# Kernel tuning notes

Hardware: AMD Instinct MI355X
Metric: run time of the kernel (lower is better)

The kernel has to match this reference:

```python
import jax, jax.numpy as jnp
import numpy as np

N, C_IN, H, W = 256, 256, 28, 28
D = 64        # prototype channel dim (prototype_shape[1])
P = 200       # num prototypes
NCLS = 10


def setup_inputs() -> dict:
    key = jax.random.key(0)
    ks = jax.random.split(key, 6)
    x = jax.random.normal(ks[0], (N, C_IN, H, W), dtype=jnp.float32)
    W1 = jax.random.normal(ks[1], (D, C_IN), dtype=jnp.float32) * 0.05
    b1 = jnp.zeros((D,), dtype=jnp.float32)
    W2 = jax.random.normal(ks[2], (D, D), dtype=jnp.float32) * 0.05
    b2 = jnp.zeros((D,), dtype=jnp.float32)
    prototypes = jax.random.uniform(ks[3], (P, D), dtype=jnp.float32)
    last_W = jax.random.normal(ks[4], (NCLS, P), dtype=jnp.float32) * 0.05
    last_b = jnp.zeros((NCLS,), dtype=jnp.float32)
    return {"x": x, "W1": W1, "b1": b1, "W2": W2, "b2": b2,
            "prototypes": prototypes, "last_W": last_W, "last_b": last_b}


def reference(x, W1, b1, W2, b2, prototypes, last_W, last_b):
    # add_on_layers: 1x1 conv -> relu -> 1x1 conv -> sigmoid (pointwise GEMMs)
    h = jax.nn.relu(jnp.einsum('nchw,oc->nohw', x, W1) + b1[None, :, None, None])
    f = jax.nn.sigmoid(jnp.einsum('nchw,oc->nohw', h, W2) + b2[None, :, None, None])
    # L2 convolution with 1x1 prototypes:
    # conv(x^2, ones) == channel sum of f^2, broadcast over P prototypes
    x2_patch_sum = jnp.sum(f * f, axis=1, keepdims=True)          # (N,1,H,W)
    xp = jnp.einsum('nchw,pc->nphw', f, prototypes)               # (N,P,H,W)
    p2 = jnp.sum(prototypes * prototypes, axis=1)[None, :, None, None]  # (1,P,1,1)
    distances = jax.nn.relu(x2_patch_sum - 2.0 * xp + p2)         # (N,P,H,W)
    # global min-pool over spatial dims (== -maxpool(-d) with full kernel)
    min_distances = jnp.min(distances, axis=(2, 3))               # (N,P)
    # paf == 'linear': similarity = -distance
    prototype_activations = -min_distances
    logits = prototype_activations @ last_W.T + last_b            # (N,NCLS)
    return (logits, min_distances)
```

## Files before the change

### kernel.cpp

```cpp
#include <hip/hip_runtime.h>
#include <hip/hip_bf16.h>

#define NIMG 256
#define CIN  256
#define PIX  784
#define DD   64
#define NP   200
#define NPP  208
#define NCLS 10

#define XS 264
#define HS 72

typedef __attribute__((ext_vector_type(8))) short bf16x8;
typedef __attribute__((ext_vector_type(4))) float f32x4;
typedef __attribute__((ext_vector_type(4))) unsigned int u32x4;
typedef __attribute__((ext_vector_type(2))) unsigned int u32x2;

__device__ __forceinline__ unsigned short f2bf(float f) {
    union { float f; unsigned int u; } v; v.f = f;
    unsigned int r = v.u + 0x7fffu + ((v.u >> 16) & 1u);
    return (unsigned short)(r >> 16);
}
__device__ __forceinline__ unsigned int pk2(float a, float b) {
    __hip_bfloat162 p = __float22bfloat162_rn(make_float2(a, b));
    return *(unsigned int*)&p;
}

#define MFMA(a, b, c) __builtin_amdgcn_mfma_f32_16x16x32_bf16((a), (b), (c), 0, 0, 0)

#define BARL() asm volatile("s_waitcnt lgkmcnt(0)\n\ts_barrier" ::: "memory")

__global__ __launch_bounds__(512, 2)
void proto_fused_kernel(const float* __restrict__ x,
                        const float* __restrict__ W1, const float* __restrict__ b1,
                        const float* __restrict__ W2, const float* __restrict__ b2,
                        const float* __restrict__ proto,
                        const float* __restrict__ lastW, const float* __restrict__ lastb,
                        float* __restrict__ out)
{
    __shared__ __align__(16) unsigned short xlds[64 * XS];
    __shared__ __align__(16) unsigned short w1lds[64 * XS];
    __shared__ __align__(16) unsigned short w2lds[64 * HS];
    __shared__ __align__(16) unsigned short htile[64 * HS];
    __shared__ __align__(16) unsigned short ftile[64 * HS];
    __shared__ float p2lds[NPP];
    __shared__ float s2lds[2][64];
    __shared__ float b1lds[DD], b2lds[DD];
    __shared__ unsigned int bmin[NPP];

    const int n    = blockIdx.x;
    const int t    = threadIdx.x;
    const int lane = t & 63;
    const int q    = lane >> 4;
    const int l15  = lane & 15;
    const int wave = t >> 6;
    const int s    = wave & 3;
    const int dh   = wave >> 2;
    const int dt0  = dh * 2, dt1 = dh * 2 + 1;

    const int p4   = ((t >> 2) & 15) * 4;
    const int c8i  = (t & 3) | ((t >> 6) << 2);
    const int c8   = c8i * 8;
    const float* xn = x + (size_t)n * CIN * PIX;

    float4 pf[8];
    auto load_tile = [&](int px0) {
        #pragma unroll
        for (int j = 0; j < 8; ++j) {
            const float* src = xn + (size_t)(c8 + j) * PIX + px0 + p4;
            float4 v;
            if (px0 + p4 + 3 < PIX) {
                v = *(const float4*)src;
            } else {
                v.x = (px0 + p4 + 0 < PIX) ? src[0] : 0.f;
                v.y = (px0 + p4 + 1 < PIX) ? src[1] : 0.f;
                v.z = (px0 + p4 + 2 < PIX) ? src[2] : 0.f;
                v.w = (px0 + p4 + 3 < PIX) ? src[3] : 0.f;
            }
            pf[j] = v;
        }
    };
    auto store_tile = [&]() {
        #pragma unroll
        for (int r = 0; r < 4; ++r) {
            u32x4 uv;
            uv.x = pk2(((const float*)&pf[0])[r], ((const float*)&pf[1])[r]);
            uv.y = pk2(((const float*)&pf[2])[r], ((const float*)&pf[3])[r]);
            uv.z = pk2(((const float*)&pf[4])[r], ((const float*)&pf[5])[r]);
            uv.w = pk2(((const float*)&pf[6])[r], ((const float*)&pf[7])[r]);
            *(u32x4*)&xlds[(p4 + r) * XS + c8] = uv;
        }
    };

    load_tile(0);

    {
        const float4* W1v = (const float4*)W1;
        #pragma unroll
        for (int i = 0; i < 8; ++i) {
            int j = t + i * 512;
            float4 v = W1v[j];
            u32x2 w;
            w.x = pk2(v.x, v.y); w.y = pk2(v.z, v.w);
            *(u32x2*)&w1lds[(j >> 6) * XS + (j & 63) * 4] = w;
        }
    }
    {
        const float4* W2v = (const float4*)W2;
        #pragma unroll
        for (int i = 0; i < 2; ++i) {
            int j = t + i * 512;
            float4 v = W2v[j];
            u32x2 w;
            w.x = pk2(v.x, v.y); w.y = pk2(v.z, v.w);
            *(u32x2*)&w2lds[(j >> 4) * HS + (j & 15) * 4] = w;
        }
    }
    if (t < DD) { b1lds[t] = b1[t]; b2lds[t] = b2[t]; }
    if (t < NPP) {
        float acc = 0.f;
        if (t < NP) {
            const float4* pp = (const float4*)(proto + t * DD);
            #pragma unroll
            for (int i = 0; i < 16; ++i) {
                float4 v = pp[i];
                acc += v.x * v.x + v.y * v.y + v.z * v.z + v.w * v.w;
            }
        }
        p2lds[t] = acc;
        bmin[t] = 0x7f800000u;
    }

    bf16x8 pb0[7], pb1[7];
    #pragma unroll
    for (int it = 0; it < 7; ++it) {
        int pt = dh + 2 * it;
        int p  = pt * 16 + l15;
        int pr = (p < NP) ? p : (NP - 1);
        const float4* src = (const float4*)(proto + (size_t)pr * DD + q * 8);
        float4 a = src[0], b = src[1];
        float4 c = src[8], d = src[9];
        union { u32x4 u; bf16x8 h; } cv0, cv1;
        cv0.u.x = pk2(a.x, a.y); cv0.u.y = pk2(a.z, a.w);
        cv0.u.z = pk2(b.x, b.y); cv0.u.w = pk2(b.z, b.w);
        cv1.u.x = pk2(c.x, c.y); cv1.u.y = pk2(c.z, c.w);
        cv1.u.z = pk2(d.x, d.y); cv1.u.w = pk2(d.z, d.w);
        pb0[it] = cv0.h; pb1[it] = cv1.h;
    }

    store_tile();
    load_tile(64);
    BARL();

    bf16x8 w1f0[8], w1f1[8];
    #pragma unroll
    for (int kk = 0; kk < 8; ++kk) {
        w1f0[kk] = *(const bf16x8*)&w1lds[(dt0 * 16 + l15) * XS + kk * 32 + q * 8];
        w1f1[kk] = *(const bf16x8*)&w1lds[(dt1 * 16 + l15) * XS + kk * 32 + q * 8];
    }
    bf16x8 w2f0[2], w2f1[2];
    #pragma unroll
    for (int kk = 0; kk < 2; ++kk) {
        w2f0[kk] = *(const bf16x8*)&w2lds[(dt0 * 16 + l15) * HS + kk * 32 + q * 8];
        w2f1[kk] = *(const bf16x8*)&w2lds[(dt1 * 16 + l15) * HS + kk * 32 + q * 8];
    }
    float p2r[7];
    #pragma unroll
    for (int it = 0; it < 7; ++it) {
        int pidx = (dh + 2 * it) * 16 + l15;
        p2r[it] = p2lds[pidx < NPP ? pidx : (NPP - 1)];
    }

    float rmin[7];
    #pragma unroll
    for (int it = 0; it < 7; ++it) rmin[it] = 1e30f;

    for (int tl = 0; tl < 13; ++tl) {
        const int px0 = tl * 64;

        {
            f32x4 acc0 = {0.f, 0.f, 0.f, 0.f}, acc1 = {0.f, 0.f, 0.f, 0.f};
            const int arow = (s * 16 + l15) * XS + q * 8;
            #pragma unroll
            for (int kk = 0; kk < 8; ++kk) {
                bf16x8 a = *(const bf16x8*)&xlds[arow + kk * 32];
                acc0 = MFMA(a, w1f0[kk], acc0);
                acc1 = MFMA(a, w1f1[kk], acc1);
            }
            #pragma unroll
            for (int r = 0; r < 4; ++r) {
                int prow = s * 16 + q * 4 + r;
                float h0 = fmaxf(acc0[r] + b1lds[dt0 * 16 + l15], 0.f);
                float h1 = fmaxf(acc1[r] + b1lds[dt1 * 16 + l15], 0.f);
                htile[prow * HS + dt0 * 16 + l15] = f2bf(h0);
                htile[prow * HS + dt1 * 16 + l15] = f2bf(h1);
            }
        }
        BARL();

        if (tl < 12) store_tile();
        if (tl < 11) load_tile((tl + 2) * 64);
        {
            f32x4 acc0 = {0.f, 0.f, 0.f, 0.f}, acc1 = {0.f, 0.f, 0.f, 0.f};
            const int arowH = (s * 16 + l15) * HS + q * 8;
            bf16x8 a0 = *(const bf16x8*)&htile[arowH];
            bf16x8 a1 = *(const bf16x8*)&htile[arowH + 32];
            acc0 = MFMA(a0, w2f0[0], acc0);
            acc0 = MFMA(a1, w2f0[1], acc0);
            acc1 = MFMA(a0, w2f1[0], acc1);
            acc1 = MFMA(a1, w2f1[1], acc1);
            #pragma unroll
            for (int r = 0; r < 4; ++r) {
                int prow = s * 16 + q * 4 + r;
                float z0 = acc0[r] + b2lds[dt0 * 16 + l15];
                float z1 = acc1[r] + b2lds[dt1 * 16 + l15];
                float f0 = __builtin_amdgcn_rcpf(1.0f + __builtin_amdgcn_exp2f(z0 * -1.44269504f));
                float f1 = __builtin_amdgcn_rcpf(1.0f + __builtin_amdgcn_exp2f(z1 * -1.44269504f));
                ftile[prow * HS + dt0 * 16 + l15] = f2bf(f0);
                ftile[prow * HS + dt1 * 16 + l15] = f2bf(f1);
                float v = f0 * f0 + f1 * f1;
                v += __shfl_xor(v, 1, 64);
                v += __shfl_xor(v, 2, 64);
                v += __shfl_xor(v, 4, 64);
                v += __shfl_xor(v, 8, 64);
                if (l15 == 0)
                    s2lds[dh][prow] = (px0 + prow < PIX) ? v : 1e30f;
            }
        }
        BARL();

        {
            const int arowF = (s * 16 + l15) * HS + q * 8;
            bf16x8 a0 = *(const bf16x8*)&ftile[arowF];
            bf16x8 a1 = *(const bf16x8*)&ftile[arowF + 32];
            float s2v[4];
            #pragma unroll
            for (int r = 0; r < 4; ++r) {
                int pl = s * 16 + q * 4 + r;
                s2v[r] = s2lds[0][pl] + s2lds[1][pl];
            }
            #pragma unroll
            for (int it = 0; it < 7; ++it) {
                f32x4 acc = {0.f, 0.f, 0.f, 0.f};
                acc = MFMA(a0, pb0[it], acc);
                acc = MFMA(a1, pb1[it], acc);
                float m = 1e30f;
                #pragma unroll
                for (int r = 0; r < 4; ++r) {
                    float dist = fmaxf(s2v[r] - 2.f * acc[r] + p2r[it], 0.f);
                    m = fminf(m, dist);
                }
                rmin[it] = fminf(rmin[it], m);
            }
        }
    }

    #pragma unroll
    for (int it = 0; it < 7; ++it) {
        int pt = dh + 2 * it;
        if (pt < 13) {
            float m = rmin[it];
            m = fminf(m, __shfl_xor(m, 16, 64));
            m = fminf(m, __shfl_xor(m, 32, 64));
            if (lane < 16) atomicMin(&bmin[pt * 16 + l15], __float_as_uint(m));
        }
    }
    BARL();

    if (t < NP) {
        out[NIMG * NCLS + (size_t)n * NP + t] = __uint_as_float(bmin[t]);
    }
    if (t < 320) {
        int c = t >> 5, j = t & 31;
        float acc = 0.f;
        for (int p = j; p < NP; p += 32)
            acc += __uint_as_float(bmin[p]) * lastW[c * NP + p];
        acc += __shfl_xor(acc, 1, 32);
        acc += __shfl_xor(acc, 2, 32);
        acc += __shfl_xor(acc, 4, 32);
        acc += __shfl_xor(acc, 8, 32);
        acc += __shfl_xor(acc, 16, 32);
        if (j == 0) out[(size_t)n * NCLS + c] = -acc + lastb[c];
    }
}

extern "C" void kernel_launch(void* const* d_in, const int* in_sizes, int n_in,
                              void* d_out, int out_size, void* d_ws, size_t ws_size,
                              hipStream_t stream) {
    const float* x     = (const float*)d_in[0];
    const float* W1    = (const float*)d_in[1];
    const float* b1    = (const float*)d_in[2];
    const float* W2    = (const float*)d_in[3];
    const float* b2    = (const float*)d_in[4];
    const float* proto = (const float*)d_in[5];
    const float* lastW = (const float*)d_in[6];
    const float* lastb = (const float*)d_in[7];
    float* out = (float*)d_out;

    proto_fused_kernel<<<dim3(NIMG), dim3(512), 0, stream>>>(
        x, W1, b1, W2, b2, proto, lastW, lastb, out);
}
```

Before: 307.2 us.

## Stage x tiles in 128-pixel double chunks and stream W1 fragments from LDS

The x staging buffer grows to two 64-pixel halves and each global prefetch now covers 128 pixels (16 float4 registers), stored every other sub-tile, so loads have a longer window to overlap compute. To free the registers this needs, the W1 MFMA fragments are no longer held in registers and are instead reread from LDS on every sub-tile. This adds LDS traffic and doubles the shared-memory footprint of xlds, which could hurt occupancy at two blocks per CU. It also leaves the stored half untouched until the next store, relying on barrier ordering between halves.

```diff
diff --git a/kernel.cpp b/kernel.cpp
--- a/kernel.cpp
+++ b/kernel.cpp
@@ -39,7 +39,7 @@
                         const float* __restrict__ lastW, const float* __restrict__ lastb,
                         float* __restrict__ out)
 {
-    __shared__ __align__(16) unsigned short xlds[64 * XS];
+    __shared__ __align__(16) unsigned short xlds[128 * XS];
     __shared__ __align__(16) unsigned short w1lds[64 * XS];
     __shared__ __align__(16) unsigned short w2lds[64 * HS];
     __shared__ __align__(16) unsigned short htile[64 * HS];
@@ -64,36 +64,44 @@
     const int c8   = c8i * 8;
     const float* xn = x + (size_t)n * CIN * PIX;
 
-    float4 pf[8];
-    auto load_tile = [&](int px0) {
+    float4 pf[16];
+    auto load_tile128 = [&](int h) {
+        const int px0 = h * 128;
         #pragma unroll
         for (int j = 0; j < 8; ++j) {
-            const float* src = xn + (size_t)(c8 + j) * PIX + px0 + p4;
-            float4 v;
-            if (px0 + p4 + 3 < PIX) {
-                v = *(const float4*)src;
-            } else {
-                v.x = (px0 + p4 + 0 < PIX) ? src[0] : 0.f;
-                v.y = (px0 + p4 + 1 < PIX) ? src[1] : 0.f;
-                v.z = (px0 + p4 + 2 < PIX) ? src[2] : 0.f;
-                v.w = (px0 + p4 + 3 < PIX) ? src[3] : 0.f;
-            }
-            pf[j] = v;
+            #pragma unroll
+            for (int half = 0; half < 2; ++half) {
+                const int base = px0 + half * 64 + p4;
+                const float* src = xn + (size_t)(c8 + j) * PIX + base;
+                float4 v;
+                if (base + 3 < PIX) {
+                    v = *(const float4*)src;
+                } else {
+                    v.x = (base + 0 < PIX) ? src[0] : 0.f;
+                    v.y = (base + 1 < PIX) ? src[1] : 0.f;
+                    v.z = (base + 2 < PIX) ? src[2] : 0.f;
+                    v.w = (base + 3 < PIX) ? src[3] : 0.f;
+                }
+                pf[j * 2 + half] = v;
+            }
         }
     };
-    auto store_tile = [&]() {
+    auto store_tile128 = [&]() {
         #pragma unroll
-        for (int r = 0; r < 4; ++r) {
-            u32x4 uv;
-            uv.x = pk2(((const float*)&pf[0])[r], ((const float*)&pf[1])[r]);
-            uv.y = pk2(((const float*)&pf[2])[r], ((const float*)&pf[3])[r]);
-            uv.z = pk2(((const float*)&pf[4])[r], ((const float*)&pf[5])[r]);
-            uv.w = pk2(((const float*)&pf[6])[r], ((const float*)&pf[7])[r]);
-            *(u32x4*)&xlds[(p4 + r) * XS + c8] = uv;
+        for (int half = 0; half < 2; ++half) {
+            #pragma unroll
+            for (int r = 0; r < 4; ++r) {
+                u32x4 uv;
+                uv.x = pk2(((const float*)&pf[0 + half])[r], ((const float*)&pf[2 + half])[r]);
+                uv.y = pk2(((const float*)&pf[4 + half])[r], ((const float*)&pf[6 + half])[r]);
+                uv.z = pk2(((const float*)&pf[8 + half])[r], ((const float*)&pf[10 + half])[r]);
+                uv.w = pk2(((const float*)&pf[12 + half])[r], ((const float*)&pf[14 + half])[r]);
+                *(u32x4*)&xlds[(half * 64 + p4 + r) * XS + c8] = uv;
+            }
         }
     };
 
-    load_tile(0);
+    load_tile128(0);
 
     {
         const float4* W1v = (const float4*)W1;
@@ -149,16 +157,10 @@
         pb0[it] = cv0.h; pb1[it] = cv1.h;
     }
 
-    store_tile();
-    load_tile(64);
+    store_tile128();
+    load_tile128(1);
     BARL();
 
-    bf16x8 w1f0[8], w1f1[8];
-    #pragma unroll
-    for (int kk = 0; kk < 8; ++kk) {
-        w1f0[kk] = *(const bf16x8*)&w1lds[(dt0 * 16 + l15) * XS + kk * 32 + q * 8];
-        w1f1[kk] = *(const bf16x8*)&w1lds[(dt1 * 16 + l15) * XS + kk * 32 + q * 8];
-    }
     bf16x8 w2f0[2], w2f1[2];
     #pragma unroll
     for (int kk = 0; kk < 2; ++kk) {
@@ -176,17 +178,23 @@
     #pragma unroll
     for (int it = 0; it < 7; ++it) rmin[it] = 1e30f;
 
-    for (int tl = 0; tl < 13; ++tl) {
-        const int px0 = tl * 64;
+    const int w1r0 = (dt0 * 16 + l15) * XS + q * 8;
+    const int w1r1 = (dt1 * 16 + l15) * XS + q * 8;
+
+    for (int st = 0; st < 13; ++st) {
+        const int px0   = st * 64;
+        const int rbase = (st & 1) * 64;
 
         {
             f32x4 acc0 = {0.f, 0.f, 0.f, 0.f}, acc1 = {0.f, 0.f, 0.f, 0.f};
-            const int arow = (s * 16 + l15) * XS + q * 8;
+            const int arow = (rbase + s * 16 + l15) * XS + q * 8;
             #pragma unroll
             for (int kk = 0; kk < 8; ++kk) {
-                bf16x8 a = *(const bf16x8*)&xlds[arow + kk * 32];
-                acc0 = MFMA(a, w1f0[kk], acc0);
-                acc1 = MFMA(a, w1f1[kk], acc1);
+                bf16x8 a  = *(const bf16x8*)&xlds[arow + kk * 32];
+                bf16x8 w0 = *(const bf16x8*)&w1lds[w1r0 + kk * 32];
+                bf16x8 w1v = *(const bf16x8*)&w1lds[w1r1 + kk * 32];
+                acc0 = MFMA(a, w0, acc0);
+                acc1 = MFMA(a, w1v, acc1);
             }
             #pragma unroll
             for (int r = 0; r < 4; ++r) {
@@ -199,8 +207,10 @@
         }
         BARL();
 
-        if (tl < 12) store_tile();
-        if (tl < 11) load_tile((tl + 2) * 64);
+        if (st & 1) {
+            store_tile128();
+            if (st <= 9) load_tile128((st >> 1) + 2);
+        }
         {
             f32x4 acc0 = {0.f, 0.f, 0.f, 0.f}, acc1 = {0.f, 0.f, 0.f, 0.f};
             const int arowH = (s * 16 + l15) * HS + q * 8;
```

Result: no change. 312.1 us (+1.6%).

## Double block to 1024 threads with four-wave D split and deeper x prefetch

Applied to the files above, without the earlier changes.

Each block now runs 16 waves instead of 8. Each wave owns one 16-channel D tile instead of two, and the prototype tiles are spread over four wave groups instead of two. The x tile load is split into a three-buffer, deeper register prefetch rotation. W2 fragments are loaded straight from global memory into registers, and W1 fragments are re-read from LDS every iteration to save registers. The aim is more latency hiding on each CU, since a 256-image grid gives one block per CU. The cost is extra LDS traffic, a wider barrier and some waves idling in the prototype stage.

```diff
diff --git a/kernel.cpp b/kernel.cpp
--- a/kernel.cpp
+++ b/kernel.cpp
@@ -31,7 +31,7 @@
 
 #define BARL() asm volatile("s_waitcnt lgkmcnt(0)\n\ts_barrier" ::: "memory")
 
-__global__ __launch_bounds__(512, 2)
+__global__ __launch_bounds__(1024)
 void proto_fused_kernel(const float* __restrict__ x,
                         const float* __restrict__ W1, const float* __restrict__ b1,
                         const float* __restrict__ W2, const float* __restrict__ b2,
@@ -41,11 +41,10 @@
 {
     __shared__ __align__(16) unsigned short xlds[64 * XS];
     __shared__ __align__(16) unsigned short w1lds[64 * XS];
-    __shared__ __align__(16) unsigned short w2lds[64 * HS];
     __shared__ __align__(16) unsigned short htile[64 * HS];
     __shared__ __align__(16) unsigned short ftile[64 * HS];
     __shared__ float p2lds[NPP];
-    __shared__ float s2lds[2][64];
+    __shared__ float s2lds[4][64];
     __shared__ float b1lds[DD], b2lds[DD];
     __shared__ unsigned int bmin[NPP];
 
@@ -56,65 +55,54 @@
     const int l15  = lane & 15;
     const int wave = t >> 6;
     const int s    = wave & 3;
-    const int dh   = wave >> 2;
-    const int dt0  = dh * 2, dt1 = dh * 2 + 1;
-
-    const int p4   = ((t >> 2) & 15) * 4;
-    const int c8i  = (t & 3) | ((t >> 6) << 2);
-    const int c8   = c8i * 8;
+    const int dt   = wave >> 2;
+
+    const int p4  = ((t >> 2) & 15) * 4;
+    const int c4i = (t & 3) | ((t >> 6) << 2);
+    const int c4  = c4i * 4;
     const float* xn = x + (size_t)n * CIN * PIX;
 
-    float4 pf[8];
-    auto load_tile = [&](int px0) {
+    auto load_st = [&](float4 (&pf)[4], int st) {
+        const int base = st * 64 + p4;
         #pragma unroll
-        for (int j = 0; j < 8; ++j) {
-            const float* src = xn + (size_t)(c8 + j) * PIX + px0 + p4;
+        for (int j = 0; j < 4; ++j) {
+            const float* src = xn + (size_t)(c4 + j) * PIX + base;
             float4 v;
-            if (px0 + p4 + 3 < PIX) {
+            if (base + 3 < PIX) {
                 v = *(const float4*)src;
             } else {
-                v.x = (px0 + p4 + 0 < PIX) ? src[0] : 0.f;
-                v.y = (px0 + p4 + 1 < PIX) ? src[1] : 0.f;
-                v.z = (px0 + p4 + 2 < PIX) ? src[2] : 0.f;
-                v.w = (px0 + p4 + 3 < PIX) ? src[3] : 0.f;
+                v.x = (base + 0 < PIX) ? src[0] : 0.f;
+                v.y = (base + 1 < PIX) ? src[1] : 0.f;
+                v.z = (base + 2 < PIX) ? src[2] : 0.f;
+                v.w = (base + 3 < PIX) ? src[3] : 0.f;
             }
             pf[j] = v;
         }
     };
-    auto store_tile = [&]() {
+    auto store_st = [&](float4 (&pf)[4]) {
         #pragma unroll
         for (int r = 0; r < 4; ++r) {
-            u32x4 uv;
-            uv.x = pk2(((const float*)&pf[0])[r], ((const float*)&pf[1])[r]);
-            uv.y = pk2(((const float*)&pf[2])[r], ((const float*)&pf[3])[r]);
-            uv.z = pk2(((const float*)&pf[4])[r], ((const float*)&pf[5])[r]);
-            uv.w = pk2(((const float*)&pf[6])[r], ((const float*)&pf[7])[r]);
-            *(u32x4*)&xlds[(p4 + r) * XS + c8] = uv;
+            u32x2 w;
+            w.x = pk2(((const float*)&pf[0])[r], ((const float*)&pf[1])[r]);
+            w.y = pk2(((const float*)&pf[2])[r], ((const float*)&pf[3])[r]);
+            *(u32x2*)&xlds[(p4 + r) * XS + c4] = w;
         }
     };
 
-    load_tile(0);
+    float4 pfA[4], pfB[4], pfC[4];
+    load_st(pfA, 0);
+    load_st(pfB, 1);
+    load_st(pfC, 2);
 
     {
         const float4* W1v = (const float4*)W1;
         #pragma unroll
-        for (int i = 0; i < 8; ++i) {
-            int j = t + i * 512;
+        for (int i = 0; i < 4; ++i) {
+            int j = t + i * 1024;
             float4 v = W1v[j];
             u32x2 w;
             w.x = pk2(v.x, v.y); w.y = pk2(v.z, v.w);
             *(u32x2*)&w1lds[(j >> 6) * XS + (j & 63) * 4] = w;
-        }
-    }
-    {
-        const float4* W2v = (const float4*)W2;
-        #pragma unroll
-        for (int i = 0; i < 2; ++i) {
-            int j = t + i * 512;
-            float4 v = W2v[j];
-            u32x2 w;
-            w.x = pk2(v.x, v.y); w.y = pk2(v.z, v.w);
-            *(u32x2*)&w2lds[(j >> 4) * HS + (j & 15) * 4] = w;
         }
     }
     if (t < DD) { b1lds[t] = b1[t]; b2lds[t] = b2[t]; }
@@ -132,10 +120,21 @@
         bmin[t] = 0x7f800000u;
     }
 
-    bf16x8 pb0[7], pb1[7];
-    #pragma unroll
-    for (int it = 0; it < 7; ++it) {
-        int pt = dh + 2 * it;
+    bf16x8 w2f[2];
+    #pragma unroll
+    for (int kk = 0; kk < 2; ++kk) {
+        const float4* src = (const float4*)(W2 + (size_t)(dt * 16 + l15) * DD + kk * 32 + q * 8);
+        float4 a = src[0], b = src[1];
+        union { u32x4 u; bf16x8 h; } cv;
+        cv.u.x = pk2(a.x, a.y); cv.u.y = pk2(a.z, a.w);
+        cv.u.z = pk2(b.x, b.y); cv.u.w = pk2(b.z, b.w);
+        w2f[kk] = cv.h;
+    }
+
+    bf16x8 pb0[4], pb1[4];
+    #pragma unroll
+    for (int it = 0; it < 4; ++it) {
+        int pt = dt + 4 * it;
         int p  = pt * 16 + l15;
         int pr = (p < NP) ? p : (NP - 1);
         const float4* src = (const float4*)(proto + (size_t)pr * DD + q * 8);
@@ -149,116 +148,108 @@
         pb0[it] = cv0.h; pb1[it] = cv1.h;
     }
 
-    store_tile();
-    load_tile(64);
+    store_st(pfA);
+    load_st(pfA, 3);
     BARL();
 
-    bf16x8 w1f0[8], w1f1[8];
-    #pragma unroll
-    for (int kk = 0; kk < 8; ++kk) {
-        w1f0[kk] = *(const bf16x8*)&w1lds[(dt0 * 16 + l15) * XS + kk * 32 + q * 8];
-        w1f1[kk] = *(const bf16x8*)&w1lds[(dt1 * 16 + l15) * XS + kk * 32 + q * 8];
-    }
-    bf16x8 w2f0[2], w2f1[2];
-    #pragma unroll
-    for (int kk = 0; kk < 2; ++kk) {
-        w2f0[kk] = *(const bf16x8*)&w2lds[(dt0 * 16 + l15) * HS + kk * 32 + q * 8];
-        w2f1[kk] = *(const bf16x8*)&w2lds[(dt1 * 16 + l15) * HS + kk * 32 + q * 8];
-    }
-    float p2r[7];
-    #pragma unroll
-    for (int it = 0; it < 7; ++it) {
-        int pidx = (dh + 2 * it) * 16 + l15;
+    float p2r[4];
+    #pragma unroll
+    for (int it = 0; it < 4; ++it) {
+        int pidx = (dt + 4 * it) * 16 + l15;
         p2r[it] = p2lds[pidx < NPP ? pidx : (NPP - 1)];
     }
 
-    float rmin[7];
-    #pragma unroll
-    for (int it = 0; it < 7; ++it) rmin[it] = 1e30f;
-
-    for (int tl = 0; tl < 13; ++tl) {
-        const int px0 = tl * 64;
-
+    float rmin[4];
+    #pragma unroll
+    for (int it = 0; it < 4; ++it) rmin[it] = 1e30f;
+
+    const int arow  = (s * 16 + l15) * XS + q * 8;
+    const int wrow  = (dt * 16 + l15) * XS + q * 8;
+    const int arowH = (s * 16 + l15) * HS + q * 8;
+    const int bidx  = dt * 16 + l15;
+
+    auto ITER = [&](int st, float4 (&pf)[4]) {
         {
-            f32x4 acc0 = {0.f, 0.f, 0.f, 0.f}, acc1 = {0.f, 0.f, 0.f, 0.f};
-            const int arow = (s * 16 + l15) * XS + q * 8;
+            f32x4 acc = {0.f, 0.f, 0.f, 0.f};
             #pragma unroll
             for (int kk = 0; kk < 8; ++kk) {
                 bf16x8 a = *(const bf16x8*)&xlds[arow + kk * 32];
-                acc0 = MFMA(a, w1f0[kk], acc0);
-                acc1 = MFMA(a, w1f1[kk], acc1);
+                bf16x8 w = *(const bf16x8*)&w1lds[wrow + kk * 32];
+                acc = MFMA(a, w, acc);
             }
             #pragma unroll
             for (int r = 0; r < 4; ++r) {
                 int prow = s * 16 + q * 4 + r;
-                float h0 = fmaxf(acc0[r] + b1lds[dt0 * 16 + l15], 0.f);
-                float h1 = fmaxf(acc1[r] + b1lds[dt1 * 16 + l15], 0.f);
-                htile[prow * HS + dt0 * 16 + l15] = f2bf(h0);
-                htile[prow * HS + dt1 * 16 + l15] = f2bf(h1);
+                float h = fmaxf(acc[r] + b1lds[bidx], 0.f);
+                htile[prow * HS + bidx] = f2bf(h);
             }
         }
         BARL();
 
-        if (tl < 12) store_tile();
-        if (tl < 11) load_tile((tl + 2) * 64);
+        if (st < 12) {
+            store_st(pf);
+            if (st <= 8) load_st(pf, st + 4);
+        }
         {
-            f32x4 acc0 = {0.f, 0.f, 0.f, 0.f}, acc1 = {0.f, 0.f, 0.f, 0.f};
-            const int arowH = (s * 16 + l15) * HS + q * 8;
+            f32x4 acc = {0.f, 0.f, 0.f, 0.f};
             bf16x8 a0 = *(const bf16x8*)&htile[arowH];
             bf16x8 a1 = *(const bf16x8*)&htile[arowH + 32];
-            acc0 = MFMA(a0, w2f0[0], acc0);
-            acc0 = MFMA(a1, w2f0[1], acc0);
-            acc1 = MFMA(a0, w2f1[0], acc1);
-            acc1 = MFMA(a1, w2f1[1], acc1);
+            acc = MFMA(a0, w2f[0], acc);
+            acc = MFMA(a1, w2f[1], acc);
             #pragma unroll
             for (int r = 0; r < 4; ++r) {
                 int prow = s * 16 + q * 4 + r;
-                float z0 = acc0[r] + b2lds[dt0 * 16 + l15];
-                float z1 = acc1[r] + b2lds[dt1 * 16 + l15];
-                float f0 = __builtin_amdgcn_rcpf(1.0f + __builtin_amdgcn_exp2f(z0 * -1.44269504f));
-                float f1 = __builtin_amdgcn_rcpf(1.0f + __builtin_amdgcn_exp2f(z1 * -1.44269504f));
-                ftile[prow * HS + dt0 * 16 + l15] = f2bf(f0);
-                ftile[prow * HS + dt1 * 16 + l15] = f2bf(f1);
-                float v = f0 * f0 + f1 * f1;
+                float z = acc[r] + b2lds[bidx];
+                float f = __builtin_amdgcn_rcpf(1.0f + __builtin_amdgcn_exp2f(z * -1.44269504f));
+                ftile[prow * HS + bidx] = f2bf(f);
+                float v = f * f;
                 v += __shfl_xor(v, 1, 64);
                 v += __shfl_xor(v, 2, 64);
                 v += __shfl_xor(v, 4, 64);
                 v += __shfl_xor(v, 8, 64);
                 if (l15 == 0)
-                    s2lds[dh][prow] = (px0 + prow < PIX) ? v : 1e30f;
+                    s2lds[dt][prow] = (st * 64 + prow < PIX) ? v : 1e30f;
             }
         }
         BARL();
 
         {
-            const int arowF = (s * 16 + l15) * HS + q * 8;
-            bf16x8 a0 = *(const bf16x8*)&ftile[arowF];
-            bf16x8 a1 = *(const bf16x8*)&ftile[arowF + 32];
+            bf16x8 a0 = *(const bf16x8*)&ftile[arowH];
+            bf16x8 a1 = *(const bf16x8*)&ftile[arowH + 32];
             float s2v[4];
             #pragma unroll
             for (int r = 0; r < 4; ++r) {
                 int pl = s * 16 + q * 4 + r;
-                s2v[r] = s2lds[0][pl] + s2lds[1][pl];
-            }
-            #pragma unroll
-            for (int it = 0; it < 7; ++it) {
-                f32x4 acc = {0.f, 0.f, 0.f, 0.f};
-                acc = MFMA(a0, pb0[it], acc);
-                acc = MFMA(a1, pb1[it], acc);
-                float m = 1e30f;
-                #pragma unroll
-                for (int r = 0; r < 4; ++r) {
-                    float dist = fmaxf(s2v[r] - 2.f * acc[r] + p2r[it], 0.f);
-                    m = fminf(m, dist);
+                s2v[r] = (s2lds[0][pl] + s2lds[1][pl]) + (s2lds[2][pl] + s2lds[3][pl]);
+            }
+            #pragma unroll
+            for (int it = 0; it < 4; ++it) {
+                int pt = dt + 4 * it;
+                if (pt < 13) {
+                    f32x4 acc = {0.f, 0.f, 0.f, 0.f};
+                    acc = MFMA(a0, pb0[it], acc);
+                    acc = MFMA(a1, pb1[it], acc);
+                    float m = 1e30f;
+                    #pragma unroll
+                    for (int r = 0; r < 4; ++r) {
+                        float dist = fmaxf(s2v[r] - 2.f * acc[r] + p2r[it], 0.f);
+                        m = fminf(m, dist);
+                    }
+                    rmin[it] = fminf(rmin[it], m);
                 }
-                rmin[it] = fminf(rmin[it], m);
-            }
-        }
-    }
-
-    #pragma unroll
-    for (int it = 0; it < 7; ++it) {
-        int pt = dh + 2 * it;
+            }
+        }
+    };
+
+    for (int base = 0; base < 15; base += 3) {
+        if (base + 0 < 13) ITER(base + 0, pfB);
+        if (base + 1 < 13) ITER(base + 1, pfC);
+        if (base + 2 < 13) ITER(base + 2, pfA);
+    }
+
+    #pragma unroll
+    for (int it = 0; it < 4; ++it) {
+        int pt = dt + 4 * it;
         if (pt < 13) {
             float m = rmin[it];
             m = fminf(m, __shfl_xor(m, 16, 64));
@@ -298,6 +289,6 @@
     const float* lastb = (const float*)d_in[7];
     float* out = (float*)d_out;
 
-    proto_fused_kernel<<<dim3(NIMG), dim3(512), 0, stream>>>(
+    proto_fused_kernel<<<dim3(NIMG), dim3(1024), 0, stream>>>(
         x, W1, b1, W2, b2, proto, lastW, lastb, out);
 }
```

Measured after the change: 350.7 us. 14.2% more time.
